# Performance work log

Hardware: AMD Instinct MI355X
Metric: run time of the kernel (lower is better)

Reference implementation:

```python
import jax, jax.numpy as jnp
import numpy as np

N = 50000
IN_FEAT = 128
HIDDEN = 128
NUM_CLASS = 64
E = 1600000


def setup_inputs() -> dict:
    key = jax.random.key(0)
    ks = jax.random.split(key, 10)
    s = 1.0 / np.sqrt(HIDDEN)
    return {
        "x": jax.random.normal(ks[0], (N, IN_FEAT), dtype=jnp.float32),
        "edge_index": jax.random.randint(ks[1], (2, E), 0, N, dtype=jnp.int64),
        "We": jax.random.uniform(ks[2], (IN_FEAT, HIDDEN), jnp.float32, -s, s),
        "be": jax.random.uniform(ks[3], (HIDDEN,), jnp.float32, -s, s),
        "W1": jax.random.uniform(ks[4], (HIDDEN, HIDDEN), jnp.float32, -s, s),
        "b1": jax.random.uniform(ks[5], (HIDDEN,), jnp.float32, -s, s),
        "W2": jax.random.uniform(ks[6], (HIDDEN, HIDDEN), jnp.float32, -s, s),
        "b2": jax.random.uniform(ks[7], (HIDDEN,), jnp.float32, -s, s),
        "Wo": jax.random.uniform(ks[8], (HIDDEN, NUM_CLASS), jnp.float32, -s, s),
        "bo": jax.random.uniform(ks[9], (NUM_CLASS,), jnp.float32, -s, s),
    }


def _gcn_conv(h, src, dst, norm, W, b, n):
    # h: [N, H]; src/dst/norm: [E+N] (self-loops appended); GCNConv math:
    # out = scatter_add(norm * (h @ W)[src] -> dst) + b
    h = h @ W
    msg = h[src] * norm[:, None]  # gather + scale  [E+N, H]
    out = jax.ops.segment_sum(msg, dst, num_segments=n)
    return out + b


def reference(x, edge_index, We, be, W1, b1, W2, b2, Wo, bo):
    n = x.shape[0]
    loops = jnp.arange(n, dtype=edge_index.dtype)
    src = jnp.concatenate([edge_index[0], loops])
    dst = jnp.concatenate([edge_index[1], loops])
    # symmetric normalization D^{-1/2} (A+I) D^{-1/2}
    deg = jax.ops.segment_sum(jnp.ones_like(dst, dtype=x.dtype), dst, num_segments=n)
    dinv = jnp.where(deg > 0, jax.lax.rsqrt(deg), 0.0)
    norm = dinv[src] * dinv[dst]

    h = x @ We + be                       # encoder
    h = jax.nn.relu(_gcn_conv(h, src, dst, norm, W1, b1, n))
    h = jax.nn.relu(_gcn_conv(h, src, dst, norm, W2, b2, n))
    return h @ Wo + bo                    # decoder
```

## Files before the change

### kernel.cpp

```cpp
#include <hip/hip_runtime.h>
#include <hip/hip_fp16.h>


#define WS_ALIGN(x) (((x) + 255) & ~(size_t)255)
#define RS 100
#define BCHUNK 8192

typedef _Float16 f16x8 __attribute__((ext_vector_type(8)));
typedef float f32x4 __attribute__((ext_vector_type(4)));

__global__ void detect_zero_kernel(const unsigned* __restrict__ p, int* __restrict__ flag,
                                   unsigned* __restrict__ bfil, int nzero) {
    __shared__ int any;
    if (threadIdx.x == 0) any = 0;
    __syncthreads();
    int nz = 0;
    for (int i = threadIdx.x; i < 2048; i += blockDim.x)
        nz |= (p[2 * i + 1] != 0u) ? 1 : 0;
    if (nz) atomicOr(&any, 1);
    for (int i = threadIdx.x; i < nzero; i += blockDim.x) bfil[i] = 0u;
    __syncthreads();
    if (threadIdx.x == 0) *flag = (any == 0) ? 1 : 0;
}

__global__ __launch_bounds__(256) void bucket_kernel(
    const void* __restrict__ ep, const int* __restrict__ flag,
    unsigned* __restrict__ bkt, unsigned* __restrict__ bfill_pad,
    int E, int nbuck, int capB) {
    __shared__ unsigned lcnt[512];
    __shared__ unsigned gcur[512];
    const int tid = threadIdx.x;
    for (int i = tid; i < nbuck; i += 256) lcnt[i] = 0;
    __syncthreads();
    const int base = blockIdx.x * BCHUNK;
    const int end = min(base + BCHUNK, E);
    const int i64 = *flag;
    if (i64) {
        const long long* p = (const long long*)ep;
        for (int i = base + tid; i < end; i += 256) {
            int d = (int)p[(size_t)E + i];
            atomicAdd(&lcnt[d / RS], 1u);
        }
    } else {
        const int* p = (const int*)ep;
        for (int i = base + tid; i < end; i += 256) {
            int d = p[(size_t)E + i];
            atomicAdd(&lcnt[d / RS], 1u);
        }
    }
    __syncthreads();
    for (int i = tid; i < nbuck; i += 256)
        gcur[i] = atomicAdd(&bfill_pad[i << 4], lcnt[i]);
    __syncthreads();
    if (i64) {
        const long long* p = (const long long*)ep;
        for (int i = base + tid; i < end; i += 256) {
            int s = (int)p[i];
            int d = (int)p[(size_t)E + i];
            int part = d / RS;
            int ld = d - part * RS;
            unsigned pos = atomicAdd(&gcur[part], 1u);
            if (pos < (unsigned)capB)
                bkt[(size_t)part * capB + pos] = ((unsigned)ld << 24) | (unsigned)s;
        }
    } else {
        const int* p = (const int*)ep;
        for (int i = base + tid; i < end; i += 256) {
            int s = p[i];
            int d = p[(size_t)E + i];
            int part = d / RS;
            int ld = d - part * RS;
            unsigned pos = atomicAdd(&gcur[part], 1u);
            if (pos < (unsigned)capB)
                bkt[(size_t)part * capB + pos] = ((unsigned)ld << 24) | (unsigned)s;
        }
    }
}

__global__ __launch_bounds__(512) void bucket_scan_kernel(
    const unsigned* __restrict__ bfill_pad, unsigned* __restrict__ ebase,
    int* __restrict__ rowp, int nbuck, int capB, int n) {
    __shared__ unsigned lds[512];
    const int tid = threadIdx.x;
    unsigned v = 0;
    if (tid < nbuck) {
        v = bfill_pad[tid << 4];
        if (v > (unsigned)capB) v = capB;
    }
    lds[tid] = v;
    __syncthreads();
    for (int off = 1; off < 512; off <<= 1) {
        unsigned add = (tid >= off) ? lds[tid - off] : 0;
        __syncthreads();
        lds[tid] += add;
        __syncthreads();
    }
    if (tid < nbuck) ebase[tid] = lds[tid] - v;
    if (tid == 511) rowp[n] = (int)lds[511];
}

__global__ __launch_bounds__(256) void csr_from_bucket_kernel(
    const unsigned* __restrict__ bkt, const unsigned* __restrict__ bfill_pad,
    const unsigned* __restrict__ ebase,
    int* __restrict__ rowp, float* __restrict__ dinv, int* __restrict__ col,
    int capB, int n) {
    __shared__ unsigned hist[RS];
    __shared__ int fillo[RS];
    const int p = blockIdx.x;
    const int tid = threadIdx.x;
    for (int i = tid; i < RS; i += 256) hist[i] = 0;
    __syncthreads();
    unsigned cnt = bfill_pad[p << 4];
    if (cnt > (unsigned)capB) cnt = capB;
    const unsigned* bp = bkt + (size_t)p * capB;
    for (unsigned e = tid; e < cnt; e += 256)
        atomicAdd(&hist[bp[e] >> 24], 1u);
    __syncthreads();
    if (tid == 0) {
        int run = (int)ebase[p];
        for (int i = 0; i < RS; ++i) { fillo[i] = run; run += (int)hist[i]; }
    }
    __syncthreads();
    const int lo = p * RS;
    for (int i = tid; i < RS; i += 256) {
        int node = lo + i;
        if (node < n) {
            rowp[node] = fillo[i];
            dinv[node] = rsqrtf((float)(hist[i] + 1u));
        }
    }
    __syncthreads();
    for (unsigned e = tid; e < cnt; e += 256) {
        unsigned u = bp[e];
        int ld = (int)(u >> 24);
        int pos = atomicAdd(&fillo[ld], 1);
        col[pos] = (int)(u & 0xFFFFFFu);
    }
}

__global__ __launch_bounds__(256) void wcomb_kernel(
    const float* __restrict__ We, const float* __restrict__ W1,
    const float* __restrict__ be, float* __restrict__ Wcomb,
    float* __restrict__ bcomb) {
    int t = blockIdx.x * 256 + threadIdx.x;
    int r = t >> 7, c = t & 127;
    float s = 0.f;
    for (int k = 0; k < 128; ++k) s = fmaf(We[r * 128 + k], W1[k * 128 + c], s);
    Wcomb[t] = s;
    if (t < 128) {
        float b = 0.f;
        for (int k = 0; k < 128; ++k) b = fmaf(be[k], W1[k * 128 + t], b);
        bcomb[t] = b;
    }
}

__global__ __launch_bounds__(256) void wfrag3_kernel(
    const float* __restrict__ Wa, __half* __restrict__ WaF,
    const float* __restrict__ Wb, __half* __restrict__ WbF,
    const float* __restrict__ Wc, __half* __restrict__ WcF, int nco) {
    const float* W;
    __half* Wf;
    int ncol, t;
    if (blockIdx.x < 8)       { W = Wa; Wf = WaF; ncol = 128; t = blockIdx.x * 256 + threadIdx.x; }
    else if (blockIdx.x < 16) { W = Wb; Wf = WbF; ncol = 128; t = (blockIdx.x - 8) * 256 + threadIdx.x; }
    else                      { W = Wc; Wf = WcF; ncol = nco; t = (blockIdx.x - 16) * 256 + threadIdx.x; }
    int total = (ncol >> 4) * 4 * 64;
    if (t >= total) return;
    int lane = t & 63;
    int ks = (t >> 6) & 3;
    int c0 = t >> 8;
    int colw = c0 * 16 + (lane & 15);
    int k0 = ks * 32 + ((lane >> 4) << 3);
    __half vals[8];
#pragma unroll
    for (int j = 0; j < 8; ++j) vals[j] = __float2half(W[(size_t)(k0 + j) * ncol + colw]);
    *(uint4*)(Wf + (size_t)t * 8) = *(uint4*)vals;
}

__global__ __launch_bounds__(256) void agg_pull_kernel(
    const int* __restrict__ rowp, const int* __restrict__ col,
    const float* __restrict__ dinv, const __half* __restrict__ t,
    const float* __restrict__ bias, __half* __restrict__ out, int n) {
    int node = blockIdx.x * 8 + (threadIdx.x >> 5);
    int lane = threadIdx.x & 31;
    if (node >= n) return;
    const uint2* T = (const uint2*)t;
    int j0 = rowp[node], j1 = rowp[node + 1];
    float dn = dinv[node];

    uint2 sraw = T[(size_t)node * 32 + lane];
    float2 s01 = __half22float2(*(const __half2*)&sraw.x);
    float2 s23 = __half22float2(*(const __half2*)&sraw.y);
    float4 acc = make_float4(s01.x, s01.y, s23.x, s23.y);

    int j = j0;
    for (; j + 7 < j1; j += 8) {
        int c[8];
        uint2 r[8];
#pragma unroll
        for (int k = 0; k < 8; ++k) c[k] = col[j + k];
#pragma unroll
        for (int k = 0; k < 8; ++k) r[k] = T[(size_t)c[k] * 32 + lane];
#pragma unroll
        for (int k = 0; k < 8; ++k) {
            float2 f01 = __half22float2(*(const __half2*)&r[k].x);
            float2 f23 = __half22float2(*(const __half2*)&r[k].y);
            acc.x += f01.x; acc.y += f01.y; acc.z += f23.x; acc.w += f23.y;
        }
    }
    for (; j + 3 < j1; j += 4) {
        int c[4];
        uint2 r[4];
#pragma unroll
        for (int k = 0; k < 4; ++k) c[k] = col[j + k];
#pragma unroll
        for (int k = 0; k < 4; ++k) r[k] = T[(size_t)c[k] * 32 + lane];
#pragma unroll
        for (int k = 0; k < 4; ++k) {
            float2 f01 = __half22float2(*(const __half2*)&r[k].x);
            float2 f23 = __half22float2(*(const __half2*)&r[k].y);
            acc.x += f01.x; acc.y += f01.y; acc.z += f23.x; acc.w += f23.y;
        }
    }
    for (; j < j1; ++j) {
        int c = col[j];
        uint2 raw = T[(size_t)c * 32 + lane];
        float2 f01 = __half22float2(*(const __half2*)&raw.x);
        float2 f23 = __half22float2(*(const __half2*)&raw.y);
        acc.x += f01.x; acc.y += f01.y; acc.z += f23.x; acc.w += f23.y;
    }

    float4 b = ((const float4*)bias)[lane];
    float ox = fmaxf(fmaf(acc.x, dn, b.x), 0.f);
    float oy = fmaxf(fmaf(acc.y, dn, b.y), 0.f);
    float oz = fmaxf(fmaf(acc.z, dn, b.z), 0.f);
    float ow = fmaxf(fmaf(acc.w, dn, b.w), 0.f);
    __half2 h01 = __floats2half2_rn(ox, oy);
    __half2 h23 = __floats2half2_rn(oz, ow);
    uint2 packed;
    packed.x = *(unsigned*)&h01;
    packed.y = *(unsigned*)&h23;
    ((uint2*)(out + (size_t)node * 128))[lane] = packed;
}

__device__ __forceinline__ f16x8 frag_from_f32(const float* p) {
    float4 u = *(const float4*)p;
    float4 v = *(const float4*)(p + 4);
    f16x8 r;
    r[0] = (_Float16)u.x; r[1] = (_Float16)u.y; r[2] = (_Float16)u.z; r[3] = (_Float16)u.w;
    r[4] = (_Float16)v.x; r[5] = (_Float16)v.y; r[6] = (_Float16)v.z; r[7] = (_Float16)v.w;
    return r;
}

__global__ __launch_bounds__(256) void gemm_mfma_kernel(
    const void* __restrict__ A, const __half* __restrict__ Wf,
    const float* __restrict__ bias, const float* __restrict__ rowscale,
    void* __restrict__ C, int n, int ncol, int a_fp32, int c_fp32) {
    const int wave = threadIdx.x >> 6;
    const int lane = threadIdx.x & 63;
    const int row0 = blockIdx.x * 64 + wave * 16;
    int ar = row0 + (lane & 15);
    if (ar >= n) ar = n - 1;
    const int koff = (lane >> 4) << 3;
    f16x8 a0, a1, a2, a3;
    if (a_fp32) {
        const float* ab = (const float*)A + (size_t)ar * 128 + koff;
        a0 = frag_from_f32(ab);
        a1 = frag_from_f32(ab + 32);
        a2 = frag_from_f32(ab + 64);
        a3 = frag_from_f32(ab + 96);
    } else {
        const __half* ab = (const __half*)A + (size_t)ar * 128 + koff;
        a0 = *(const f16x8*)(ab);
        a1 = *(const f16x8*)(ab + 32);
        a2 = *(const f16x8*)(ab + 64);
        a3 = *(const f16x8*)(ab + 96);
    }
    const int ncc = ncol >> 4;
    const int cic = lane & 15;
    const int rbase = (lane >> 4) << 2;
    float rs[4];
#pragma unroll
    for (int r = 0; r < 4; ++r) {
        int row = row0 + rbase + r;
        rs[r] = (rowscale && row < n) ? rowscale[row] : 1.f;
    }
    for (int c0 = 0; c0 < ncc; ++c0) {
        const f16x8* wf = (const f16x8*)Wf + (size_t)c0 * 256 + lane;
        f32x4 acc = {0.f, 0.f, 0.f, 0.f};
        acc = __builtin_amdgcn_mfma_f32_16x16x32_f16(a0, wf[0],   acc, 0, 0, 0);
        acc = __builtin_amdgcn_mfma_f32_16x16x32_f16(a1, wf[64],  acc, 0, 0, 0);
        acc = __builtin_amdgcn_mfma_f32_16x16x32_f16(a2, wf[128], acc, 0, 0, 0);
        acc = __builtin_amdgcn_mfma_f32_16x16x32_f16(a3, wf[192], acc, 0, 0, 0);
        int colc = (c0 << 4) + cic;
        float bv = bias ? bias[colc] : 0.f;
#pragma unroll
        for (int r = 0; r < 4; ++r) {
            int row = row0 + rbase + r;
            if (row < n) {
                float v = (acc[r] + bv) * rs[r];
                if (c_fp32) ((float*)C)[(size_t)row * ncol + colc] = v;
                else        ((__half*)C)[(size_t)row * ncol + colc] = __float2half(v);
            }
        }
    }
}

extern "C" void kernel_launch(void* const* d_in, const int* in_sizes, int n_in,
                              void* d_out, int out_size, void* d_ws, size_t ws_size,
                              hipStream_t stream) {
    const float* x  = (const float*)d_in[0];
    const void*  ei = d_in[1];
    const float* We = (const float*)d_in[2];
    const float* be = (const float*)d_in[3];
    const float* W1 = (const float*)d_in[4];
    const float* b1 = (const float*)d_in[5];
    const float* W2 = (const float*)d_in[6];
    const float* b2 = (const float*)d_in[7];
    const float* Wo = (const float*)d_in[8];
    const float* bo = (const float*)d_in[9];
    const int N = in_sizes[0] / 128;
    const int E = in_sizes[1] / 2;
    const int NC = in_sizes[9];
    const int nbuck = (N + RS - 1) / RS;
    const int capB = (E + nbuck - 1) / nbuck + 512;

    char* ws = (char*)d_ws;
    size_t off = 0;
    int*      flag = (int*)(ws + off);      off += 256;
    unsigned* bfil = (unsigned*)(ws + off); off += WS_ALIGN((size_t)nbuck * 64);
    unsigned* ebas = (unsigned*)(ws + off); off += WS_ALIGN((size_t)nbuck * 4);
    unsigned* bkt  = (unsigned*)(ws + off); off += WS_ALIGN((size_t)nbuck * capB * 4);
    float*    dinv = (float*)(ws + off);    off += WS_ALIGN((size_t)N * 4);
    int*      rowp = (int*)(ws + off);      off += WS_ALIGN((size_t)(N + 1) * 4);
    int*      colw = (int*)(ws + off);      off += WS_ALIGN((size_t)E * 4);
    float*    Wcmb = (float*)(ws + off);    off += WS_ALIGN((size_t)128 * 128 * 4);
    float*    bcmb = (float*)(ws + off);    off += WS_ALIGN((size_t)128 * 4);
    __half*   WcF  = (__half*)(ws + off);   off += WS_ALIGN((size_t)128 * 128 * 2);
    __half*   W2F  = (__half*)(ws + off);   off += WS_ALIGN((size_t)128 * 128 * 2);
    __half*   WoF  = (__half*)(ws + off);   off += WS_ALIGN((size_t)128 * 64 * 2);
    __half*   hA   = (__half*)(ws + off);   off += WS_ALIGN((size_t)N * 128 * 2);
    __half*   tH   = (__half*)(ws + off);   off += WS_ALIGN((size_t)N * 128 * 2);

    const int nb_bucket = (E + BCHUNK - 1) / BCHUNK;
    dim3 blk(256);

    detect_zero_kernel<<<1, 256, 0, stream>>>((const unsigned*)ei, flag, bfil, nbuck * 16);
    bucket_kernel<<<nb_bucket, blk, 0, stream>>>(ei, flag, bkt, bfil, E, nbuck, capB);
    bucket_scan_kernel<<<1, 512, 0, stream>>>(bfil, ebas, rowp, nbuck, capB, N);
    csr_from_bucket_kernel<<<nbuck, blk, 0, stream>>>(bkt, bfil, ebas, rowp, dinv, colw, capB, N);

    wcomb_kernel<<<64, blk, 0, stream>>>(We, W1, be, Wcmb, bcmb);
    wfrag3_kernel<<<20, blk, 0, stream>>>(Wcmb, WcF, W2, W2F, Wo, WoF, NC);

    const int gemm_blocks = (N + 63) / 64;
    const int agg_blocks = (N + 7) / 8;

    gemm_mfma_kernel<<<gemm_blocks, blk, 0, stream>>>(x, WcF, bcmb, dinv, tH, N, 128, 1, 0);
    agg_pull_kernel<<<agg_blocks, blk, 0, stream>>>(rowp, colw, dinv, tH, b1, hA, N);
    gemm_mfma_kernel<<<gemm_blocks, blk, 0, stream>>>(hA, W2F, nullptr, dinv, tH, N, 128, 0, 0);
    agg_pull_kernel<<<agg_blocks, blk, 0, stream>>>(rowp, colw, dinv, tH, b2, hA, N);
    gemm_mfma_kernel<<<gemm_blocks, blk, 0, stream>>>(hA, WoF, bo, nullptr, d_out, N, NC, 0, 1);
}
```

Measured before the change: 212.8 us.

## Widen aggregation gathers to 16B per lane and sort CSR columns by source chunk

The pull aggregation now gives each node 16 lanes that each load a uint4 (8 halves), where before it used 32 lanes loading uint2. This halves the number of load instructions per gathered row and packs 16 nodes into each block. The CSR build now fills column lists in 8 passes over source-index ranges, so each node's neighbours come out roughly ordered by source and gathers get better locality. The cost is rescanning each bucket 8 times, plus barriers, in the CSR build kernel.

Result: slower. 224.5 us (+5.5%).

```diff
diff --git a/kernel.cpp b/kernel.cpp
--- a/kernel.cpp
+++ b/kernel.cpp
@@ -5,6 +5,7 @@
 #define WS_ALIGN(x) (((x) + 255) & ~(size_t)255)
 #define RS 100
 #define BCHUNK 8192
+#define SCHUNKS 8
 
 typedef _Float16 f16x8 __attribute__((ext_vector_type(8)));
 typedef float f32x4 __attribute__((ext_vector_type(4)));
@@ -130,11 +131,21 @@
         }
     }
     __syncthreads();
-    for (unsigned e = tid; e < cnt; e += 256) {
-        unsigned u = bp[e];
-        int ld = (int)(u >> 24);
-        int pos = atomicAdd(&fillo[ld], 1);
-        col[pos] = (int)(u & 0xFFFFFFu);
+    const int csz = (n + SCHUNKS - 1) / SCHUNKS;
+#pragma unroll 1
+    for (int q = 0; q < SCHUNKS; ++q) {
+        int lo_s = q * csz;
+        int hi_s = lo_s + csz;
+        for (unsigned e = tid; e < cnt; e += 256) {
+            unsigned u = bp[e];
+            int s = (int)(u & 0xFFFFFFu);
+            if (s >= lo_s && s < hi_s) {
+                int ld = (int)(u >> 24);
+                int pos = atomicAdd(&fillo[ld], 1);
+                col[pos] = s;
+            }
+        }
+        __syncthreads();
     }
 }
 
@@ -177,70 +188,72 @@
     *(uint4*)(Wf + (size_t)t * 8) = *(uint4*)vals;
 }
 
+__device__ __forceinline__ void h8_acc(uint4 r, float* a) {
+    float2 f;
+    f = __half22float2(*(const __half2*)&r.x); a[0] += f.x; a[1] += f.y;
+    f = __half22float2(*(const __half2*)&r.y); a[2] += f.x; a[3] += f.y;
+    f = __half22float2(*(const __half2*)&r.z); a[4] += f.x; a[5] += f.y;
+    f = __half22float2(*(const __half2*)&r.w); a[6] += f.x; a[7] += f.y;
+}
+
 __global__ __launch_bounds__(256) void agg_pull_kernel(
     const int* __restrict__ rowp, const int* __restrict__ col,
     const float* __restrict__ dinv, const __half* __restrict__ t,
     const float* __restrict__ bias, __half* __restrict__ out, int n) {
-    int node = blockIdx.x * 8 + (threadIdx.x >> 5);
-    int lane = threadIdx.x & 31;
+    int node = blockIdx.x * 16 + (threadIdx.x >> 4);
+    int lane = threadIdx.x & 15;
     if (node >= n) return;
-    const uint2* T = (const uint2*)t;
+    const uint4* T = (const uint4*)t;
     int j0 = rowp[node], j1 = rowp[node + 1];
     float dn = dinv[node];
 
-    uint2 sraw = T[(size_t)node * 32 + lane];
-    float2 s01 = __half22float2(*(const __half2*)&sraw.x);
-    float2 s23 = __half22float2(*(const __half2*)&sraw.y);
-    float4 acc = make_float4(s01.x, s01.y, s23.x, s23.y);
+    float acc[8] = {0.f, 0.f, 0.f, 0.f, 0.f, 0.f, 0.f, 0.f};
+    h8_acc(T[(size_t)node * 16 + lane], acc);
 
     int j = j0;
     for (; j + 7 < j1; j += 8) {
         int c[8];
-        uint2 r[8];
+        uint4 r[8];
 #pragma unroll
         for (int k = 0; k < 8; ++k) c[k] = col[j + k];
 #pragma unroll
-        for (int k = 0; k < 8; ++k) r[k] = T[(size_t)c[k] * 32 + lane];
-#pragma unroll
-        for (int k = 0; k < 8; ++k) {
-            float2 f01 = __half22float2(*(const __half2*)&r[k].x);
-            float2 f23 = __half22float2(*(const __half2*)&r[k].y);
-            acc.x += f01.x; acc.y += f01.y; acc.z += f23.x; acc.w += f23.y;
-        }
+        for (int k = 0; k < 8; ++k) r[k] = T[(size_t)c[k] * 16 + lane];
+#pragma unroll
+        for (int k = 0; k < 8; ++k) h8_acc(r[k], acc);
     }
     for (; j + 3 < j1; j += 4) {
         int c[4];
-        uint2 r[4];
+        uint4 r[4];
 #pragma unroll
         for (int k = 0; k < 4; ++k) c[k] = col[j + k];
 #pragma unroll
-        for (int k = 0; k < 4; ++k) r[k] = T[(size_t)c[k] * 32 + lane];
-#pragma unroll
-        for (int k = 0; k < 4; ++k) {
-            float2 f01 = __half22float2(*(const __half2*)&r[k].x);
-            float2 f23 = __half22float2(*(const __half2*)&r[k].y);
-            acc.x += f01.x; acc.y += f01.y; acc.z += f23.x; acc.w += f23.y;
-        }
-    }
-    for (; j < j1; ++j) {
-        int c = col[j];
-        uint2 raw = T[(size_t)c * 32 + lane];
-        float2 f01 = __half22float2(*(const __half2*)&raw.x);
-        float2 f23 = __half22float2(*(const __half2*)&raw.y);
-        acc.x += f01.x; acc.y += f01.y; acc.z += f23.x; acc.w += f23.y;
-    }
-
-    float4 b = ((const float4*)bias)[lane];
-    float ox = fmaxf(fmaf(acc.x, dn, b.x), 0.f);
-    float oy = fmaxf(fmaf(acc.y, dn, b.y), 0.f);
-    float oz = fmaxf(fmaf(acc.z, dn, b.z), 0.f);
-    float ow = fmaxf(fmaf(acc.w, dn, b.w), 0.f);
-    __half2 h01 = __floats2half2_rn(ox, oy);
-    __half2 h23 = __floats2half2_rn(oz, ow);
-    uint2 packed;
-    packed.x = *(unsigned*)&h01;
-    packed.y = *(unsigned*)&h23;
-    ((uint2*)(out + (size_t)node * 128))[lane] = packed;
+        for (int k = 0; k < 4; ++k) r[k] = T[(size_t)c[k] * 16 + lane];
+#pragma unroll
+        for (int k = 0; k < 4; ++k) h8_acc(r[k], acc);
+    }
+    for (; j < j1; ++j) h8_acc(T[(size_t)col[j] * 16 + lane], acc);
+
+    const float4* B4 = (const float4*)bias;
+    float4 ba = B4[lane * 2 + 0];
+    float4 bb = B4[lane * 2 + 1];
+    float o0 = fmaxf(fmaf(acc[0], dn, ba.x), 0.f);
+    float o1 = fmaxf(fmaf(acc[1], dn, ba.y), 0.f);
+    float o2 = fmaxf(fmaf(acc[2], dn, ba.z), 0.f);
+    float o3 = fmaxf(fmaf(acc[3], dn, ba.w), 0.f);
+    float o4 = fmaxf(fmaf(acc[4], dn, bb.x), 0.f);
+    float o5 = fmaxf(fmaf(acc[5], dn, bb.y), 0.f);
+    float o6 = fmaxf(fmaf(acc[6], dn, bb.z), 0.f);
+    float o7 = fmaxf(fmaf(acc[7], dn, bb.w), 0.f);
+    __half2 h0 = __floats2half2_rn(o0, o1);
+    __half2 h1 = __floats2half2_rn(o2, o3);
+    __half2 h2 = __floats2half2_rn(o4, o5);
+    __half2 h3 = __floats2half2_rn(o6, o7);
+    uint4 packed;
+    packed.x = *(unsigned*)&h0;
+    packed.y = *(unsigned*)&h1;
+    packed.z = *(unsigned*)&h2;
+    packed.w = *(unsigned*)&h3;
+    ((uint4*)out)[(size_t)node * 16 + lane] = packed;
 }
 
 __device__ __forceinline__ f16x8 frag_from_f32(const float* p) {
@@ -354,7 +367,7 @@
     wfrag3_kernel<<<20, blk, 0, stream>>>(Wcmb, WcF, W2, W2F, Wo, WoF, NC);
 
     const int gemm_blocks = (N + 63) / 64;
-    const int agg_blocks = (N + 7) / 8;
+    const int agg_blocks = (N + 15) / 16;
 
     gemm_mfma_kernel<<<gemm_blocks, blk, 0, stream>>>(x, WcF, bcmb, dinv, tH, N, 128, 1, 0);
     agg_pull_kernel<<<agg_blocks, blk, 0, stream>>>(rowp, colw, dinv, tH, b1, hA, N);
```
